# Kernel tuning notes

Measured on AMD Instinct MI355X. Metric: run time of the kernel, lower is better.

## Reference

```python
import jax, jax.numpy as jnp
import numpy as np


def _pairwise_sq_dists(t):
    # t: [B, L, R] -> [B, L, L] squared L2 distances via ||a||^2+||b||^2-2a.b
    sq = jnp.sum(t * t, axis=-1)                      # [B, L]
    dots = jnp.einsum('bir,bjr->bij', t, t)           # [B, L, L]
    d = sq[:, :, None] + sq[:, None, :] - 2.0 * dots
    return jnp.maximum(d, 0.0)


def setup_inputs() -> dict:
    key = jax.random.key(0)
    k1, k2, k3 = jax.random.split(key, 3)
    B, L, D, H, R = 16, 1024, 1024, 1024, 128
    batch = jax.random.normal(k1, (B, L, D), dtype=jnp.float32)
    # Linear weights stored as [in, out]; small init to keep activations sane
    W1 = jax.random.normal(k2, (D, H), dtype=jnp.float32) * (1.0 / np.sqrt(D))
    b1 = jnp.zeros((H,), dtype=jnp.float32)
    W2 = jax.random.normal(k3, (H, R), dtype=jnp.float32) * (1.0 / np.sqrt(H))
    b2 = jnp.zeros((R,), dtype=jnp.float32)
    return {"batch": batch, "W1": W1, "b1": b1, "W2": W2, "b2": b2}


def reference(batch, W1, b1, W2, b2):
    # layer 1: Linear + clamp(min=0)
    h = jnp.maximum(jnp.einsum('bld,dh->blh', batch, W1) + b1, 0.0)
    # layer 2 (projection to probe rank): Linear + clamp(min=0)
    t = jnp.maximum(jnp.einsum('blh,hr->blr', h, W2) + b2, 0.0)
    # all-pairs squared distances per sentence: [B, L, L]
    return _pairwise_sq_dists(t)
```

## Files before the change

kernel.cpp:

```cpp
#include <hip/hip_runtime.h>
#include <stdint.h>

#define B_ 16
#define L_ 1024
#define D_ 1024
#define H_ 1024
#define R_ 128
#define M_ (B_ * L_)

using f32x4  = __attribute__((ext_vector_type(4))) float;
using bf16x8 = __attribute__((ext_vector_type(8))) short;

__device__ __forceinline__ short f2bf(float f) {
  uint32_t u = __builtin_bit_cast(uint32_t, f);
  u = (u + 0x7FFFu + ((u >> 16) & 1u)) >> 16;
  return (short)(uint16_t)u;
}
__device__ __forceinline__ float bf2f(uint16_t h) {
  return __builtin_bit_cast(float, (uint32_t)h << 16);
}

__device__ __forceinline__ bf16x8 lds_read_frag(const short* base, int elemOff) {
  bf16x8 r;
  const __attribute__((address_space(3))) short* p =
      (const __attribute__((address_space(3))) short*)(base) + elemOff;
  asm volatile("ds_read_b128 %0, %1" : "=v"(r) : "v"((uint32_t)(uintptr_t)p));
  return r;
}

#define CONV_BLKS 8192
#define T1B 256
#define T2B 32
__global__ void k_prep(const float* __restrict__ X, const float* __restrict__ W1,
                       const float* __restrict__ W2, short* __restrict__ Xb,
                       short* __restrict__ W1t, short* __restrict__ W2t) {
  __shared__ float s[64][65];
  const int b = blockIdx.x;
  if (b < CONV_BLKS) {
    size_t i = ((size_t)b * 256 + threadIdx.x) * 8;
    float4 a = *(const float4*)(X + i);
    float4 c = *(const float4*)(X + i + 4);
    union { short sh[8]; bf16x8 v; } o;
    o.sh[0] = f2bf(a.x); o.sh[1] = f2bf(a.y); o.sh[2] = f2bf(a.z); o.sh[3] = f2bf(a.w);
    o.sh[4] = f2bf(c.x); o.sh[5] = f2bf(c.y); o.sh[6] = f2bf(c.z); o.sh[7] = f2bf(c.w);
    *(bf16x8*)(Xb + i) = o.v;
    return;
  }
  const float* in; short* out; int K, N, bx, by;
  if (b < CONV_BLKS + T1B) {
    int t = b - CONV_BLKS; in = W1; out = W1t; K = D_; N = H_; bx = t & 15; by = t >> 4;
  } else {
    int t = b - CONV_BLKS - T1B; in = W2; out = W2t; K = H_; N = R_; bx = t & 1; by = t >> 1;
  }
  const int n0 = bx * 64, k0 = by * 64;
  const int tx = threadIdx.x & 63, tq = threadIdx.x >> 6;
#pragma unroll
  for (int j = 0; j < 16; ++j) {
    int r = j * 4 + tq;
    s[r][tx] = in[(size_t)(k0 + r) * N + (n0 + tx)];
  }
  __syncthreads();
#pragma unroll
  for (int j = 0; j < 16; ++j) {
    int r = j * 4 + tq;
    out[(size_t)(n0 + r) * K + (k0 + tx)] = f2bf(s[tx][r]);
  }
}

__device__ __forceinline__ void gemm_body_128_db(const short* __restrict__ Ap,
                                                 const short* __restrict__ Bp,
                                                 int ld, int kSteps,
                                                 short* As, short* Bs,
                                                 f32x4 (&acc)[4][4]) {
  const int tid = threadIdx.x, lane = tid & 63, wave = tid >> 6;
  const int wr = wave >> 1, wc = wave & 1;
  const int lrow = lane & 15, lk8 = (lane >> 4) * 8;
  const int srow = lane >> 2;
  const int skc  = (lane & 3) * 8;

  auto STAGE = [&](int ks, int d) {
    const int k0 = ks * 32;
#pragma unroll
    for (int c = 0; c < 2; ++c) {
      const int chunk = wave * 2 + c;
      const int row = chunk * 16 + srow;
      __builtin_amdgcn_global_load_lds(
          (const __attribute__((address_space(1))) void*)(Ap + (size_t)row * ld + (k0 + skc)),
          (__attribute__((address_space(3))) void*)(As + d * 4096 + chunk * 512 + lane * 8), 16, 0, 0);
      __builtin_amdgcn_global_load_lds(
          (const __attribute__((address_space(1))) void*)(Bp + (size_t)row * ld + (k0 + skc)),
          (__attribute__((address_space(3))) void*)(Bs + d * 4096 + chunk * 512 + lane * 8), 16, 0, 0);
    }
  };

  STAGE(0, 0);
  for (int ks = 0; ks < kSteps; ++ks) {
    const int cur = ks & 1;
    if (ks + 1 < kSteps) {
      STAGE(ks + 1, cur ^ 1);
      asm volatile("s_waitcnt vmcnt(4)" ::: "memory");
    } else {
      asm volatile("s_waitcnt vmcnt(0)" ::: "memory");
    }
    __builtin_amdgcn_s_barrier();
    asm volatile("" ::: "memory");

    bf16x8 af[4], bfr[4];
#pragma unroll
    for (int m = 0; m < 4; ++m)
      af[m] = lds_read_frag(As, cur * 4096 + (wr * 64 + m * 16 + lrow) * 32 + lk8);
#pragma unroll
    for (int n = 0; n < 4; ++n)
      bfr[n] = lds_read_frag(Bs, cur * 4096 + (wc * 64 + n * 16 + lrow) * 32 + lk8);
    asm volatile("s_waitcnt lgkmcnt(0)" ::: "memory");
    __builtin_amdgcn_sched_barrier(0);
    __builtin_amdgcn_s_setprio(1);
#pragma unroll
    for (int m = 0; m < 4; ++m)
#pragma unroll
      for (int n = 0; n < 4; ++n)
        acc[m][n] = __builtin_amdgcn_mfma_f32_16x16x32_bf16(af[m], bfr[n], acc[m][n], 0, 0, 0);
    __builtin_amdgcn_s_setprio(0);
    asm volatile("" ::: "memory");
    __builtin_amdgcn_s_barrier();
  }
}

__global__ __launch_bounds__(256)
void k_gemm1(const short* __restrict__ A, const short* __restrict__ Bt,
             const float* __restrict__ bias, short* __restrict__ C) {
  __shared__ __align__(16) short As[2 * 4096];
  __shared__ __align__(16) short Bs[2 * 4096];
  const int b = blockIdx.x;
  const int xcd = b & 7, seq = b >> 3;
  const int g = xcd + ((seq >> 6) << 3);
  const int i = seq & 63;
  const int m0 = (g * 8 + (i >> 3)) * 128;
  const int n0 = (i & 7) * 128;

  f32x4 acc[4][4] = {};
  gemm_body_128_db(A + (size_t)m0 * D_, Bt + (size_t)n0 * D_, D_, D_ / 32, As, Bs, acc);

  const int lane = threadIdx.x & 63, wave = threadIdx.x >> 6;
  const int wr = wave >> 1, wc = wave & 1;
  const int rbase = m0 + wr * 64 + (lane >> 4) * 4;
  const int cbase = n0 + wc * 64 + (lane & 15);
#pragma unroll
  for (int n = 0; n < 4; ++n) {
    const int col = cbase + n * 16;
    const float bn = bias[col];
#pragma unroll
    for (int m = 0; m < 4; ++m) {
      const int row = rbase + m * 16;
#pragma unroll
      for (int r = 0; r < 4; ++r) {
        float v = acc[m][n][r] + bn;
        C[(size_t)(row + r) * H_ + col] = f2bf(fmaxf(v, 0.f));
      }
    }
  }
}

__global__ __launch_bounds__(256)
void k_gemm2_splitk(const short* __restrict__ A, const short* __restrict__ Bt,
                    float* __restrict__ P) {
  __shared__ __align__(16) short As[2 * 4096];
  __shared__ __align__(16) short Bs[2 * 4096];
  const int m0 = blockIdx.y * 128;
  const int s  = blockIdx.z;
  const int kOff = s * (H_ / 4);

  f32x4 acc[4][4] = {};
  gemm_body_128_db(A + (size_t)m0 * H_ + kOff, Bt + kOff, H_, (H_ / 4) / 32, As, Bs, acc);

  const int lane = threadIdx.x & 63, wave = threadIdx.x >> 6;
  const int wr = wave >> 1, wc = wave & 1;
  const int rbase = wr * 64 + (lane >> 4) * 4;
  const int cbase = wc * 64 + (lane & 15);
  float* Ps = P + (size_t)s * M_ * R_ + (size_t)m0 * R_;
#pragma unroll
  for (int m = 0; m < 4; ++m)
#pragma unroll
    for (int r = 0; r < 4; ++r)
#pragma unroll
      for (int n = 0; n < 4; ++n)
        Ps[(size_t)(rbase + m * 16 + r) * R_ + cbase + n * 16] = acc[m][n][r];
}

__global__ void k_reduce2(const float* __restrict__ P, const float* __restrict__ b2,
                          short* __restrict__ T, float* __restrict__ sq) {
  const int row  = blockIdx.x * 4 + (threadIdx.x >> 6);
  const int lane = threadIdx.x & 63;
  const int c0 = lane * 2;
  float s0 = 0.f, s1 = 0.f;
#pragma unroll
  for (int s = 0; s < 4; ++s) {
    const float2 v = *(const float2*)(P + ((size_t)s * M_ + row) * R_ + c0);
    s0 += v.x; s1 += v.y;
  }
  float v0 = fmaxf(s0 + b2[c0], 0.f);
  float v1 = fmaxf(s1 + b2[c0 + 1], 0.f);
  uint32_t pk = (uint32_t)(uint16_t)f2bf(v0) | ((uint32_t)(uint16_t)f2bf(v1) << 16);
  *(uint32_t*)(T + (size_t)row * R_ + c0) = pk;
  float q = v0 * v0 + v1 * v1;
#pragma unroll
  for (int o = 32; o >= 1; o >>= 1) q += __shfl_xor(q, o, 64);
  if (lane == 0) sq[row] = q;
}

__global__ __launch_bounds__(256)
void k_pairwise(const short* __restrict__ T, const float* __restrict__ sq,
                float* __restrict__ out) {
  __shared__ __align__(16) short As[2 * 4096];
  __shared__ __align__(16) short Bs[2 * 4096];
  const int b = blockIdx.z;
  const short* Tb  = T  + (size_t)b * L_ * R_;
  const float* sqb = sq + (size_t)b * L_;
  const int m0 = blockIdx.y * 128, n0 = blockIdx.x * 128;

  f32x4 acc[4][4] = {};
  gemm_body_128_db(Tb + (size_t)m0 * R_, Tb + (size_t)n0 * R_, R_, R_ / 32, As, Bs, acc);

  const int lane = threadIdx.x & 63, wave = threadIdx.x >> 6;
  const int wr = wave >> 1, wc = wave & 1;
  const int rbase = m0 + wr * 64 + (lane >> 4) * 4;
  const int cbase = n0 + wc * 64 + (lane & 15);
  float sqj[4];
#pragma unroll
  for (int n = 0; n < 4; ++n) sqj[n] = sqb[cbase + n * 16];
#pragma unroll
  for (int m = 0; m < 4; ++m) {
#pragma unroll
    for (int r = 0; r < 4; ++r) {
      const int row = rbase + m * 16 + r;
      const float sqi = sqb[row];
      float* orow = out + ((size_t)b * L_ + row) * L_;
#pragma unroll
      for (int n = 0; n < 4; ++n) {
        float d = sqi + sqj[n] - 2.0f * acc[m][n][r];
        orow[cbase + n * 16] = fmaxf(d, 0.f);
      }
    }
  }
}

extern "C" void kernel_launch(void* const* d_in, const int* in_sizes, int n_in,
                              void* d_out, int out_size, void* d_ws, size_t ws_size,
                              hipStream_t stream) {
  const float* X  = (const float*)d_in[0];
  const float* W1 = (const float*)d_in[1];
  const float* b1 = (const float*)d_in[2];
  const float* W2 = (const float*)d_in[3];
  const float* b2 = (const float*)d_in[4];
  float* out = (float*)d_out;

  char* ws = (char*)d_ws;
  size_t off = 0;
  auto alloc = [&](size_t bytes) {
    char* p = ws + off;
    off += (bytes + 255) & ~(size_t)255;
    return p;
  };
  short* Xb  = (short*)alloc((size_t)M_ * D_ * 2);
  short* W1t = (short*)alloc((size_t)H_ * D_ * 2);
  short* Hb  = (short*)alloc((size_t)M_ * H_ * 2);
  short* W2t = (short*)alloc((size_t)R_ * H_ * 2);
  short* Tb  = (short*)alloc((size_t)M_ * R_ * 2);
  float* Sq  = (float*)alloc((size_t)M_ * 4);
  float* P   = (float*)Xb;

  k_prep<<<CONV_BLKS + T1B + T2B, 256, 0, stream>>>(X, W1, W2, Xb, W1t, W2t);
  k_gemm1<<<dim3((M_ / 128) * (H_ / 128)), 256, 0, stream>>>(Xb, W1t, b1, Hb);
  k_gemm2_splitk<<<dim3(1, M_ / 128, 4), 256, 0, stream>>>(Hb, W2t, P);
  k_reduce2<<<M_ / 4, 256, 0, stream>>>(P, b2, Tb, Sq);
  k_pairwise<<<dim3(L_ / 128, L_ / 128, B_), 256, 0, stream>>>(Tb, Sq, out);
}
```

Baseline: 204.4 us.

## Swizzle LDS tile layout and use immediate-offset ds_read in GEMM body

Global-to-LDS staging now XOR-swizzles the 16-byte k-chunk within each row by the row index, and fragment reads apply the matching swizzle, to spread ds_read_b128 accesses across LDS banks. The k-loop is unrolled by two so the double-buffer offset is a compile-time constant. Each fragment read uses a precomputed base address plus an immediate offset, which removes per-iteration address arithmetic. The unroll assumes kSteps is even, and the swizzle must match exactly between writes and reads.

```diff
diff --git a/kernel.cpp b/kernel.cpp
--- a/kernel.cpp
+++ b/kernel.cpp
@@ -20,11 +20,14 @@
   return __builtin_bit_cast(float, (uint32_t)h << 16);
 }
 
-__device__ __forceinline__ bf16x8 lds_read_frag(const short* base, int elemOff) {
+__device__ __forceinline__ uint32_t lds_addr(const short* p) {
+  return (uint32_t)(uintptr_t)(const __attribute__((address_space(3))) short*)p;
+}
+
+template <int OFF>
+__device__ __forceinline__ bf16x8 lds_read_off(uint32_t addr) {
   bf16x8 r;
-  const __attribute__((address_space(3))) short* p =
-      (const __attribute__((address_space(3))) short*)(base) + elemOff;
-  asm volatile("ds_read_b128 %0, %1" : "=v"(r) : "v"((uint32_t)(uintptr_t)p));
+  asm volatile("ds_read_b128 %0, %1 offset:%2" : "=v"(r) : "v"(addr), "n"(OFF));
   return r;
 }
 
@@ -74,9 +77,12 @@
                                                  f32x4 (&acc)[4][4]) {
   const int tid = threadIdx.x, lane = tid & 63, wave = tid >> 6;
   const int wr = wave >> 1, wc = wave & 1;
-  const int lrow = lane & 15, lk8 = (lane >> 4) * 8;
+  const int lrow = lane & 15;
   const int srow = lane >> 2;
-  const int skc  = (lane & 3) * 8;
+  const int skc  = (((lane & 3) ^ (srow & 3)) * 8);
+  const int rslot = (lane >> 4) ^ (lane & 3);
+  const uint32_t aBase = lds_addr(As) + (uint32_t)((wr * 64 + lrow) * 64 + rslot * 16);
+  const uint32_t bBase = lds_addr(Bs) + (uint32_t)((wc * 64 + lrow) * 64 + rslot * 16);
 
   auto STAGE = [&](int ks, int d) {
     const int k0 = ks * 32;
@@ -93,37 +99,43 @@
     }
   };
 
+#define GEMM_PHASE(KS_NEXT, STAGE_DST, CUROFF)                                 \
+  {                                                                            \
+    const int ksn = (KS_NEXT);                                                 \
+    if (ksn < kSteps) {                                                        \
+      STAGE(ksn, STAGE_DST);                                                   \
+      asm volatile("s_waitcnt vmcnt(4)" ::: "memory");                         \
+    } else {                                                                   \
+      asm volatile("s_waitcnt vmcnt(0)" ::: "memory");                         \
+    }                                                                          \
+    __builtin_amdgcn_s_barrier();                                              \
+    bf16x8 af[4], bfr[4];                                                      \
+    af[0]  = lds_read_off<(CUROFF) + 0>(aBase);                                \
+    af[1]  = lds_read_off<(CUROFF) + 1024>(aBase);                             \
+    af[2]  = lds_read_off<(CUROFF) + 2048>(aBase);                             \
+    af[3]  = lds_read_off<(CUROFF) + 3072>(aBase);                             \
+    bfr[0] = lds_read_off<(CUROFF) + 0>(bBase);                                \
+    bfr[1] = lds_read_off<(CUROFF) + 1024>(bBase);                             \
+    bfr[2] = lds_read_off<(CUROFF) + 2048>(bBase);                             \
+    bfr[3] = lds_read_off<(CUROFF) + 3072>(bBase);                             \
+    asm volatile("s_waitcnt lgkmcnt(0)" ::: "memory");                         \
+    __builtin_amdgcn_sched_barrier(0);                                         \
+    __builtin_amdgcn_s_setprio(1);                                             \
+    _Pragma("unroll") for (int m = 0; m < 4; ++m)                              \
+      _Pragma("unroll") for (int n = 0; n < 4; ++n)                            \
+        acc[m][n] = __builtin_amdgcn_mfma_f32_16x16x32_bf16(af[m], bfr[n],     \
+                                                            acc[m][n], 0, 0, 0); \
+    __builtin_amdgcn_s_setprio(0);                                             \
+    asm volatile("" ::: "memory");                                             \
+    __builtin_amdgcn_s_barrier();                                              \
+  }
+
   STAGE(0, 0);
-  for (int ks = 0; ks < kSteps; ++ks) {
-    const int cur = ks & 1;
-    if (ks + 1 < kSteps) {
-      STAGE(ks + 1, cur ^ 1);
-      asm volatile("s_waitcnt vmcnt(4)" ::: "memory");
-    } else {
-      asm volatile("s_waitcnt vmcnt(0)" ::: "memory");
-    }
-    __builtin_amdgcn_s_barrier();
-    asm volatile("" ::: "memory");
-
-    bf16x8 af[4], bfr[4];
-#pragma unroll
-    for (int m = 0; m < 4; ++m)
-      af[m] = lds_read_frag(As, cur * 4096 + (wr * 64 + m * 16 + lrow) * 32 + lk8);
-#pragma unroll
-    for (int n = 0; n < 4; ++n)
-      bfr[n] = lds_read_frag(Bs, cur * 4096 + (wc * 64 + n * 16 + lrow) * 32 + lk8);
-    asm volatile("s_waitcnt lgkmcnt(0)" ::: "memory");
-    __builtin_amdgcn_sched_barrier(0);
-    __builtin_amdgcn_s_setprio(1);
-#pragma unroll
-    for (int m = 0; m < 4; ++m)
-#pragma unroll
-      for (int n = 0; n < 4; ++n)
-        acc[m][n] = __builtin_amdgcn_mfma_f32_16x16x32_bf16(af[m], bfr[n], acc[m][n], 0, 0, 0);
-    __builtin_amdgcn_s_setprio(0);
-    asm volatile("" ::: "memory");
-    __builtin_amdgcn_s_barrier();
-  }
+  for (int ks = 0; ks < kSteps; ks += 2) {
+    GEMM_PHASE(ks + 1, 1, 0)
+    GEMM_PHASE(ks + 2, 0, 8192)
+  }
+#undef GEMM_PHASE
 }
 
 __global__ __launch_bounds__(256)
```

Result: faster. 199.5 us (-2.4%).
